# Optimization experiments

Measured on AMD Instinct MI355X. Metric: run time of the kernel, lower is better.

The kernel has to match this reference:

```python
import jax, jax.numpy as jnp
import numpy as np

B, T, D, C = 64, 512, 768, 31  # batch, bert seq len, hidden size, num clause boundaries


def setup_inputs() -> dict:
    key = jax.random.key(0)
    k1, k2, k3 = jax.random.split(key, 3)
    hidden_state = jax.random.normal(k1, (B, T, D), dtype=jnp.float32)
    # Strictly increasing clause-end token positions in (0, T): evenly spaced base + jitter
    step = T // (C + 1)  # 16
    base = (jnp.arange(1, C + 1) * step)[None, :]                       # [1, C]
    jitter = jax.random.randint(k2, (B, C), 0, step - 1)                # < step => strictly increasing
    clause_b = (base + jitter).astype(jnp.int32)                        # [B, C]
    w5 = jax.random.normal(k3, (D, 1), dtype=jnp.float32) * 0.02        # fc5 weight
    b5 = jnp.zeros((1,), dtype=jnp.float32)                             # fc5 bias
    return {"hidden_state": hidden_state, "clause_b": clause_b, "w5": w5, "b5": b5}


def reference(hidden_state, clause_b, w5, b5):
    # Per-clause variable-length softmax-attention pooling over BERT hidden states.
    # Segment j of batch b covers tokens [starts[b,j], ends[b,j]).
    Bq, Tq, Dq = hidden_state.shape
    scores = (hidden_state @ w5).squeeze(-1) + b5[0]                    # [B, T]  (fc5)
    starts = jnp.concatenate(
        [jnp.zeros((Bq, 1), clause_b.dtype), clause_b], axis=1)        # [B, C+1]
    ends = jnp.concatenate(
        [clause_b, jnp.full((Bq, 1), Tq, clause_b.dtype)], axis=1)     # [B, C+1]
    t = jnp.arange(Tq)
    mask = (t[None, None, :] >= starts[:, :, None]) & \
           (t[None, None, :] < ends[:, :, None])                       # [B, C+1, T]
    neg = jnp.asarray(-1e30, dtype=scores.dtype)
    s = jnp.where(mask, scores[:, None, :], neg)
    w = jax.nn.softmax(s, axis=-1)                                      # [B, C+1, T]
    doc_sents_h = jnp.einsum('bjt,btd->bjd', w, hidden_state)           # [B, C+1, D]
    return doc_sents_h
```

## Files before the change

kernel.cpp:

```cpp
#include <hip/hip_runtime.h>


#define B_ 64
#define T_ 512
#define D_ 768
#define C_ 31
#define NSEG 32

__global__ __launch_bounds__(256) void seg_softmax_pool_online(
    const float* __restrict__ hidden,
    const int*   __restrict__ clause_b,
    const float* __restrict__ w5,
    const float* __restrict__ b5,
    float*       __restrict__ out)
{
    const int wave = threadIdx.x >> 6;
    const int lane = threadIdx.x & 63;
    const int seg  = blockIdx.x * 4 + wave;
    const int b    = seg >> 5;
    const int j    = seg & 31;

    const int start = (j == 0)  ? 0  : clause_b[b * C_ + j - 1];
    const int end   = (j == C_) ? T_ : clause_b[b * C_ + j];
    const int L     = end - start;

    const int doff = 4 * lane;
    const float4 w0 = *(const float4*)(w5 + doff);
    const float4 w1 = *(const float4*)(w5 + doff + 256);
    const float4 w2 = *(const float4*)(w5 + doff + 512);
    const float bias = b5[0];

    const float* hseg = hidden + ((size_t)b * T_ + start) * D_ + doff;

    float4 a0 = make_float4(0.f, 0.f, 0.f, 0.f);
    float4 a1 = a0, a2 = a0;
    float m = -INFINITY, denom = 0.0f;

    float4 c0 = *(const float4*)(hseg);
    float4 c1 = *(const float4*)(hseg + 256);
    float4 c2 = *(const float4*)(hseg + 512);

    for (int t = 0; t < L; ++t) {
        float4 n0 = make_float4(0.f, 0.f, 0.f, 0.f), n1 = n0, n2 = n0;
        if (t + 1 < L) {
            const float* np = hseg + (size_t)(t + 1) * D_;
            n0 = *(const float4*)(np);
            n1 = *(const float4*)(np + 256);
            n2 = *(const float4*)(np + 512);
        }

        float p = c0.x * w0.x + c0.y * w0.y + c0.z * w0.z + c0.w * w0.w
                + c1.x * w1.x + c1.y * w1.y + c1.z * w1.z + c1.w * w1.w
                + c2.x * w2.x + c2.y * w2.y + c2.z * w2.z + c2.w * w2.w;
        #pragma unroll
        for (int off = 32; off > 0; off >>= 1)
            p += __shfl_xor(p, off, 64);
        const float s = p + bias;

        const float mn    = fmaxf(m, s);
        const float scale = __expf(m - mn);
        const float e     = __expf(s - mn);
        denom = denom * scale + e;
        a0.x = a0.x * scale + e * c0.x;  a0.y = a0.y * scale + e * c0.y;
        a0.z = a0.z * scale + e * c0.z;  a0.w = a0.w * scale + e * c0.w;
        a1.x = a1.x * scale + e * c1.x;  a1.y = a1.y * scale + e * c1.y;
        a1.z = a1.z * scale + e * c1.z;  a1.w = a1.w * scale + e * c1.w;
        a2.x = a2.x * scale + e * c2.x;  a2.y = a2.y * scale + e * c2.y;
        a2.z = a2.z * scale + e * c2.z;  a2.w = a2.w * scale + e * c2.w;
        m = mn;
        c0 = n0; c1 = n1; c2 = n2;
    }

    const float inv = 1.0f / denom;
    float* op = out + ((size_t)b * NSEG + j) * D_ + doff;
    *(float4*)(op)       = make_float4(a0.x * inv, a0.y * inv, a0.z * inv, a0.w * inv);
    *(float4*)(op + 256) = make_float4(a1.x * inv, a1.y * inv, a1.z * inv, a1.w * inv);
    *(float4*)(op + 512) = make_float4(a2.x * inv, a2.y * inv, a2.z * inv, a2.w * inv);
}

extern "C" void kernel_launch(void* const* d_in, const int* in_sizes, int n_in,
                              void* d_out, int out_size, void* d_ws, size_t ws_size,
                              hipStream_t stream) {
    const float* hidden   = (const float*)d_in[0];
    const int*   clause_b = (const int*)d_in[1];
    const float* w5       = (const float*)d_in[2];
    const float* b5       = (const float*)d_in[3];
    float*       out      = (float*)d_out;

    seg_softmax_pool_online<<<B_ * NSEG / 4, 256, 0, stream>>>(hidden, clause_b, w5, b5, out);
}
```

Measured before the change: 161.3 us.

## Split each segment's tokens across four waves and merge online-softmax partials

Each block now handles one segment instead of four. Its four waves take interleaved tokens and keep separate online-softmax states. The partial max, denominator and accumulators are then merged through shared memory and written out. This shortens the serial per-wave dependency chain, since the old grid had only 512 blocks of 4 waves each working through about 16 tokens in sequence, and exposes more memory-level parallelism. The cost is two barriers, 12KB of LDS per block and a reduction pass. When a segment has fewer than 4 tokens, some waves carry m=-inf, and __expf(-inf - M) returns 0, which is fine.

```diff
diff --git a/kernel.cpp b/kernel.cpp
--- a/kernel.cpp
+++ b/kernel.cpp
@@ -7,16 +7,17 @@
 #define C_ 31
 #define NSEG 32
 
-__global__ __launch_bounds__(256) void seg_softmax_pool_online(
+__global__ __launch_bounds__(256) void seg_softmax_pool_split(
     const float* __restrict__ hidden,
     const int*   __restrict__ clause_b,
     const float* __restrict__ w5,
     const float* __restrict__ b5,
     float*       __restrict__ out)
 {
-    const int wave = threadIdx.x >> 6;
-    const int lane = threadIdx.x & 63;
-    const int seg  = blockIdx.x * 4 + wave;
+    const int tid  = threadIdx.x;
+    const int wave = tid >> 6;
+    const int lane = tid & 63;
+    const int seg  = blockIdx.x;
     const int b    = seg >> 5;
     const int j    = seg & 31;
 
@@ -36,14 +37,18 @@
     float4 a1 = a0, a2 = a0;
     float m = -INFINITY, denom = 0.0f;
 
-    float4 c0 = *(const float4*)(hseg);
-    float4 c1 = *(const float4*)(hseg + 256);
-    float4 c2 = *(const float4*)(hseg + 512);
+    float4 c0 = a0, c1 = a0, c2 = a0;
+    if (wave < L) {
+        const float* p0 = hseg + (size_t)wave * D_;
+        c0 = *(const float4*)(p0);
+        c1 = *(const float4*)(p0 + 256);
+        c2 = *(const float4*)(p0 + 512);
+    }
 
-    for (int t = 0; t < L; ++t) {
+    for (int t = wave; t < L; t += 4) {
         float4 n0 = make_float4(0.f, 0.f, 0.f, 0.f), n1 = n0, n2 = n0;
-        if (t + 1 < L) {
-            const float* np = hseg + (size_t)(t + 1) * D_;
+        if (t + 4 < L) {
+            const float* np = hseg + (size_t)(t + 4) * D_;
             n0 = *(const float4*)(np);
             n1 = *(const float4*)(np + 256);
             n2 = *(const float4*)(np + 512);
@@ -71,11 +76,31 @@
         c0 = n0; c1 = n1; c2 = n2;
     }
 
-    const float inv = 1.0f / denom;
-    float* op = out + ((size_t)b * NSEG + j) * D_ + doff;
-    *(float4*)(op)       = make_float4(a0.x * inv, a0.y * inv, a0.z * inv, a0.w * inv);
-    *(float4*)(op + 256) = make_float4(a1.x * inv, a1.y * inv, a1.z * inv, a1.w * inv);
-    *(float4*)(op + 512) = make_float4(a2.x * inv, a2.y * inv, a2.z * inv, a2.w * inv);
+    __shared__ float s_acc[4][D_];
+    __shared__ float s_m[4], s_d[4];
+
+    if (lane == 0) { s_m[wave] = m; s_d[wave] = denom; }
+    __syncthreads();
+
+    const float M = fmaxf(fmaxf(s_m[0], s_m[1]), fmaxf(s_m[2], s_m[3]));
+    const float Tden = s_d[0] * __expf(s_m[0] - M) + s_d[1] * __expf(s_m[1] - M)
+                     + s_d[2] * __expf(s_m[2] - M) + s_d[3] * __expf(s_m[3] - M);
+    const float myscale = __expf(m - M);
+
+    float* dst = &s_acc[wave][doff];
+    *(float4*)(dst)       = make_float4(a0.x * myscale, a0.y * myscale, a0.z * myscale, a0.w * myscale);
+    *(float4*)(dst + 256) = make_float4(a1.x * myscale, a1.y * myscale, a1.z * myscale, a1.w * myscale);
+    *(float4*)(dst + 512) = make_float4(a2.x * myscale, a2.y * myscale, a2.z * myscale, a2.w * myscale);
+    __syncthreads();
+
+    const float inv = 1.0f / Tden;
+    float* op = out + ((size_t)b * NSEG + j) * D_;
+    #pragma unroll
+    for (int k = 0; k < 3; ++k) {
+        const int d = tid + k * 256;
+        const float v = s_acc[0][d] + s_acc[1][d] + s_acc[2][d] + s_acc[3][d];
+        op[d] = v * inv;
+    }
 }
 
 extern "C" void kernel_launch(void* const* d_in, const int* in_sizes, int n_in,
@@ -87,5 +112,5 @@
     const float* b5       = (const float*)d_in[3];
     float*       out      = (float*)d_out;
 
-    seg_softmax_pool_online<<<B_ * NSEG / 4, 256, 0, stream>>>(hidden, clause_b, w5, b5, out);
+    seg_softmax_pool_split<<<B_ * NSEG, 256, 0, stream>>>(hidden, clause_b, w5, b5, out);
 }
```

Result: faster. 155.8 us (median of 2 runs) (-3.4%).
